# Kernel tuning notes

Measured on AMD Instinct MI355X. Metric: run time of the kernel, lower is better.

The kernel has to match this reference:

```python
import jax, jax.numpy as jnp
import numpy as np
from jax import lax

PATCH_NUM = 84      # MultiHeadSelector default
SCALE = 0.7         # scaling_factor for non-selected patches
KERNEL = jnp.array([[1., 2., 1.], [2., 4., 2.], [1., 2., 1.]], dtype=jnp.float32).reshape(1, 1, 3, 3)


def setup_inputs() -> dict:
    key = jax.random.key(0)
    k1, k2, k3, k4 = jax.random.split(key, 4)
    B, C, S, D = 8, 12, 784, 768   # batch, heads, patches (28x28), hidden
    N = S + 1
    hidden_states = jax.random.normal(k1, (B, N, D), jnp.float32)
    x = jax.random.normal(k2, (B, C, N, N), jnp.float32)          # attention weights
    s1 = 1.0 / np.sqrt(512).astype(np.float32)
    s2 = 1.0 / np.sqrt(D).astype(np.float32)
    gcn_w1 = jax.random.uniform(k3, (2, 512), jnp.float32, -s1, s1)
    gcn_w2 = jax.random.uniform(k4, (512, D), jnp.float32, -s2, s2)
    return {"hidden_states": hidden_states, "x": x, "gcn_w1": gcn_w1, "gcn_w2": gcn_w2, "select_num": 42}


def reference(hidden_states, x, gcn_w1, gcn_w2, select_num):
    B, C, N = x.shape[0], x.shape[1], x.shape[2]
    S = N - 1
    H = int(np.sqrt(S))
    # ---- top-k patch selection per head, rescale non-selected scores ----
    score = x[:, :, 0, 1:]                                   # [B,C,S] CLS->patch attn
    _, sel_idx = lax.top_k(score, PATCH_NUM)                 # [B,C,K]
    bi = jnp.arange(B)[:, None, None]
    ci = jnp.arange(C)[None, :, None]
    select = jnp.zeros(score.shape, bool).at[bi, ci, sel_idx].set(True)
    new_score = jnp.where(select, score, score * SCALE)
    amap = new_score.reshape(B, C, H, H)                     # attention map
    # ---- RelativeCoordPredictor ----
    m = amap.sum(axis=1).reshape(B, S)
    binary = (m > m.mean(axis=1, keepdims=True)).astype(amap.dtype)
    masked = (amap * binary.reshape(B, 1, H, H)).reshape(B, C, S).transpose(0, 2, 1)  # [B,S,C]
    anchor_idx = jnp.argmax(masked.mean(axis=-1), axis=-1)   # [B]
    ii, jj = jnp.meshgrid(jnp.arange(H), jnp.arange(H), indexing='ij')
    label = jnp.stack([ii, jj], -1).reshape(S, 2).astype(amap.dtype)  # [S,2] (i,j) coords
    anchor = label[anchor_idx]                               # [B,2]
    rc = (label[None, :, :] - anchor[:, None, :]) / H
    dist = jnp.sqrt((rc ** 2).sum(-1))
    ang = (jnp.arctan2(rc[:, :, 1], rc[:, :, 0]) / np.pi + 1.0) / 2.0
    structure_info = jnp.stack([dist, ang], -1)              # [B,S,2]
    pw = amap.reshape(B, C, S).transpose(0, 2, 1).mean(-1)   # [B,S]
    adj = pw[:, :, None] * pw[:, None, :]                    # [B,S,S] position weight
    # ---- GCN (eval mode; dropout off). relu(leaky_relu(x)) == relu(x). ----
    h1 = jnp.maximum(jnp.einsum('bst,btk->bsk', adj, structure_info @ gcn_w1), 0)
    o2 = jnp.einsum('bst,btk->bsk', adj, h1 @ gcn_w2)
    struct = jnp.where(o2 > 0, o2, 0.2 * o2)                 # [B,S,D]
    # ---- per-sample anchor injection into CLS token ----
    hs = hidden_states.at[:, 0].add(struct[jnp.arange(B), anchor_idx])
    # ---- vote counts across heads (bincount), local 3x3 enhancement ----
    count = jnp.zeros((B, S), hs.dtype).at[jnp.arange(B)[:, None], sel_idx.reshape(B, -1)].add(1.0)
    count = lax.conv_general_dilated(count.reshape(B, 1, H, H), KERNEL.astype(hs.dtype), (1, 1), 'SAME',
                                     dimension_numbers=('NCHW', 'OIHW', 'NCHW')).reshape(B, S)
    order = jnp.argsort(-count, axis=-1, stable=True)        # descending sort
    patch_idx = order[:, :select_num] + 1                    # +1 skips CLS token
    selected = hs[jnp.arange(B)[:, None], patch_idx]         # [B,select_num,D]
    return hs, selected
```

## Files before the change

### kernel.cpp

```cpp
#include <hip/hip_runtime.h>
#include <math.h>

#define Bz 8
#define Cc 12
#define Ss 784
#define Nn 785
#define Dd 768
#define Hh 28
#define K1 512
#define PATCHNUM 84

__device__ inline float waveSum(float v) {
#pragma unroll
    for (int off = 32; off > 0; off >>= 1) v += __shfl_xor(v, off);
    return v;
}

__global__ __launch_bounds__(256) void kA_score(const float* __restrict__ x,
                                                float* __restrict__ nscore,
                                                unsigned char* __restrict__ flags) {
    int bc = blockIdx.x;
    int quarter = blockIdx.y;
    int tid = threadIdx.x;
    const float* sc = x + (size_t)bc * Nn * Nn + 1;
    __shared__ float s_sc[Ss];
    for (int s = tid; s < Ss; s += 256) s_sc[s] = sc[s];
    __syncthreads();

    int s = tid + 256 * quarter;
    bool valid = (s < Ss);
    float v = valid ? s_sc[s] : 0.f;
    int rank = 0;
    const float4* s4 = (const float4*)s_sc;
    for (int chunk = 0; chunk < Ss / 16; ++chunk) {
        float4 c0 = s4[chunk * 4 + 0];
        float4 c1 = s4[chunk * 4 + 1];
        float4 c2 = s4[chunk * 4 + 2];
        float4 c3 = s4[chunk * 4 + 3];
        float c[16] = {c0.x, c0.y, c0.z, c0.w, c1.x, c1.y, c1.z, c1.w,
                       c2.x, c2.y, c2.z, c2.w, c3.x, c3.y, c3.z, c3.w};
#pragma unroll
        for (int u = 0; u < 16; ++u) {
            int t = chunk * 16 + u;
            rank += (c[u] > v) || (c[u] == v && t < s);
        }
    }
    if (valid) {
        bool sel = rank < PATCHNUM;
        flags[(size_t)bc * Ss + s] = sel ? 1 : 0;
        nscore[(size_t)bc * Ss + s] = sel ? v : v * 0.7f;
    }
}

__global__ __launch_bounds__(256) void kMid(const float* __restrict__ nscore,
                                            const unsigned char* __restrict__ flags,
                                            const float* __restrict__ w1,
                                            const float* __restrict__ w2,
                                            float* __restrict__ pbuf,
                                            int* __restrict__ selpos, int select_num) {
    int bid = blockIdx.x;
    int tid = threadIdx.x;
    int wid = tid >> 6, lane = tid & 63;

    if (bid < 192) {
        int b = bid / 24;
        int r = bid % 24;
        int kb = r / 3, colblk = r % 3;
        __shared__ float s_m[Ss];
        __shared__ float s_pw[Ss];
        __shared__ float s_g[64];
        __shared__ float s_w1[4];
        __shared__ float s_w4[4][4];
        __shared__ float s_av[4];
        __shared__ int   s_ai[4];

        const float* ns = nscore + (size_t)b * Cc * Ss;
        float lsum = 0.f;
        for (int s = tid; s < Ss; s += 256) {
            float m = 0.f;
#pragma unroll
            for (int c = 0; c < Cc; ++c) m += ns[c * Ss + s];
            s_m[s] = m;
            s_pw[s] = m / 12.0f;
            lsum += m;
        }
        lsum = waveSum(lsum);
        if (lane == 0) s_w1[wid] = lsum;
        __syncthreads();
        float meanm = (s_w1[0] + s_w1[1] + s_w1[2] + s_w1[3]) / 784.0f;

        float bv = -INFINITY; int bi = Ss;
        for (int s = tid; s < Ss; s += 256) {
            float z = (s_m[s] > meanm) ? s_pw[s] : 0.0f;
            if (z > bv) { bv = z; bi = s; }
        }
#pragma unroll
        for (int off = 32; off > 0; off >>= 1) {
            float ov = __shfl_xor(bv, off);
            int   oi = __shfl_xor(bi, off);
            if (ov > bv || (ov == bv && oi < bi)) { bv = ov; bi = oi; }
        }
        if (lane == 0) { s_av[wid] = bv; s_ai[wid] = bi; }
        __syncthreads();
        float abv = s_av[0]; int anchor = s_ai[0];
#pragma unroll
        for (int w = 1; w < 4; ++w) {
            if (s_av[w] > abv || (s_av[w] == abv && s_ai[w] < anchor)) {
                abv = s_av[w]; anchor = s_ai[w];
            }
        }

        int ai = anchor / Hh, aj = anchor % Hh;
        float lA = 0.f, lG = 0.f, lp = 0.f, ln2 = 0.f;
        const float PI_F = 3.14159265358979323846f;
        for (int s = tid; s < Ss; s += 256) {
            float pw = s_pw[s];
            int i = s / Hh, j = s % Hh;
            float ri = (float)(i - ai) / 28.0f;
            float rj = (float)(j - aj) / 28.0f;
            float dist = sqrtf(ri * ri + rj * rj);
            float ang = (atan2f(rj, ri) / PI_F + 1.0f) * 0.5f;
            lA += pw * dist;
            lG += pw * ang;
            if (pw > 0.f) lp += pw * pw;
            else if (pw < 0.f) ln2 += pw * pw;
        }
        lA = waveSum(lA); lG = waveSum(lG); lp = waveSum(lp); ln2 = waveSum(ln2);
        if (lane == 0) {
            s_w4[wid][0] = lA; s_w4[wid][1] = lG; s_w4[wid][2] = lp; s_w4[wid][3] = ln2;
        }
        __syncthreads();
        float A   = s_w4[0][0] + s_w4[1][0] + s_w4[2][0] + s_w4[3][0];
        float G   = s_w4[0][1] + s_w4[1][1] + s_w4[2][1] + s_w4[3][1];
        float P2p = s_w4[0][2] + s_w4[1][2] + s_w4[2][2] + s_w4[3][2];
        float P2n = s_w4[0][3] + s_w4[1][3] + s_w4[2][3] + s_w4[3][3];
        float pwA = s_pw[anchor];
        float cp = pwA * P2p, cn = pwA * P2n;

        if (tid < 64) {
            int k = kb * 64 + tid;
            float v = A * w1[k] + G * w1[K1 + k];
            s_g[tid] = cp * fmaxf(v, 0.f) - cn * fmaxf(-v, 0.f);
        }
        __syncthreads();

        int col = colblk * 256 + tid;
        float acc = 0.f;
        const float* w2p = w2 + (size_t)(kb * 64) * Dd + col;
#pragma unroll 8
        for (int kk = 0; kk < 64; ++kk)
            acc += s_g[kk] * w2p[kk * Dd];
        pbuf[((size_t)kb * Bz + b) * Dd + col] = acc;
    } else {
        int u = bid - 192;
        int b = u / 4;
        int quarter = u % 4;
        __shared__ int s_cnt[Ss];
        __shared__ int s_cc[Ss];
        for (int s = tid; s < Ss; s += 256) {
            int c0 = 0;
#pragma unroll
            for (int c = 0; c < Cc; ++c) c0 += flags[((size_t)b * Cc + c) * Ss + s];
            s_cnt[s] = c0;
        }
        __syncthreads();
        for (int s = tid; s < Ss; s += 256) {
            int i = s / Hh, j = s % Hh;
            int acc = 0;
            for (int di = -1; di <= 1; ++di)
                for (int dj = -1; dj <= 1; ++dj) {
                    int ii = i + di, jj = j + dj;
                    if (ii >= 0 && ii < Hh && jj >= 0 && jj < Hh)
                        acc += ((di == 0) ? 2 : 1) * ((dj == 0) ? 2 : 1) * s_cnt[ii * Hh + jj];
                }
            s_cc[s] = acc;
        }
        __syncthreads();
        int s = tid + 256 * quarter;
        int v = 0, rank = 0;
        bool valid = (s < Ss);
        if (valid) v = s_cc[s];
        const int4* s4 = (const int4*)s_cc;
        for (int chunk = 0; chunk < Ss / 16; ++chunk) {
            int4 c0 = s4[chunk * 4 + 0];
            int4 c1 = s4[chunk * 4 + 1];
            int4 c2 = s4[chunk * 4 + 2];
            int4 c3 = s4[chunk * 4 + 3];
            int c[16] = {c0.x, c0.y, c0.z, c0.w, c1.x, c1.y, c1.z, c1.w,
                         c2.x, c2.y, c2.z, c2.w, c3.x, c3.y, c3.z, c3.w};
#pragma unroll
            for (int u2 = 0; u2 < 16; ++u2) {
                int t = chunk * 16 + u2;
                rank += (c[u2] > v) || (c[u2] == v && t < s);
            }
        }
        if (valid && rank < select_num)
            selpos[b * select_num + rank] = s + 1;
    }
}

__global__ __launch_bounds__(256) void kE_out(const float* __restrict__ hs,
                                              const float* __restrict__ pbuf,
                                              const int* __restrict__ selpos,
                                              float* __restrict__ out,
                                              int select_num, int blocksCopy) {
    int bid = blockIdx.x;
    if (bid < blocksCopy) {
        size_t v = (size_t)bid * 256 + threadIdx.x;
        size_t total = (size_t)Bz * Nn * Dd / 4;
        if (v >= total) return;
        float4 val = ((const float4*)hs)[v];
        size_t fidx = v * 4;
        int b = (int)(fidx / ((size_t)Nn * Dd));
        int r = (int)(fidx % ((size_t)Nn * Dd));
        if (r < Dd) {
            float4 o2 = make_float4(0.f, 0.f, 0.f, 0.f);
#pragma unroll
            for (int kb = 0; kb < 8; ++kb) {
                float4 p = *(const float4*)(pbuf + ((size_t)kb * Bz + b) * Dd + r);
                o2.x += p.x; o2.y += p.y; o2.z += p.z; o2.w += p.w;
            }
            val.x += (o2.x > 0.f) ? o2.x : 0.2f * o2.x;
            val.y += (o2.y > 0.f) ? o2.y : 0.2f * o2.y;
            val.z += (o2.z > 0.f) ? o2.z : 0.2f * o2.z;
            val.w += (o2.w > 0.f) ? o2.w : 0.2f * o2.w;
        }
        ((float4*)out)[v] = val;
    } else {
        int v = (bid - blocksCopy) * 256 + threadIdx.x;
        int total = Bz * select_num * Dd / 4;
        if (v >= total) return;
        int fidx = v * 4;
        int b = fidx / (select_num * Dd);
        int r = fidx % (select_num * Dd);
        int p = r / Dd;
        int d = r % Dd;
        int row = selpos[b * select_num + p];
        float4 val = *(const float4*)(hs + ((size_t)b * Nn + row) * Dd + d);
        ((float4*)(out + (size_t)Bz * Nn * Dd))[v] = val;
    }
}

extern "C" void kernel_launch(void* const* d_in, const int* in_sizes, int n_in,
                              void* d_out, int out_size, void* d_ws, size_t ws_size,
                              hipStream_t stream) {
    const float* hs = (const float*)d_in[0];
    const float* x  = (const float*)d_in[1];
    const float* w1 = (const float*)d_in[2];
    const float* w2 = (const float*)d_in[3];
    float* out = (float*)d_out;

    const int hsN = Bz * Nn * Dd;
    int select_num = (out_size - hsN) / (Bz * Dd);

    char* ws = (char*)d_ws;
    float* nscore = (float*)ws;
    unsigned char* flags = (unsigned char*)(ws + 301056);
    float* pbuf  = (float*)(ws + 376320);
    int* selpos  = (int*)(ws + 572928);

    kA_score<<<dim3(Bz * Cc, 4), 256, 0, stream>>>(x, nscore, flags);
    kMid<<<224, 256, 0, stream>>>(nscore, flags, w1, w2, pbuf, selpos, select_num);

    int blocksCopy = (hsN / 4 + 255) / 256;
    int selTotal = Bz * select_num * Dd / 4;
    int blocksGather = (selTotal + 255) / 256;
    kE_out<<<blocksCopy + blocksGather, 256, 0, stream>>>(hs, pbuf, selpos, out,
                                                          select_num, blocksCopy);
}
```

Measured before the change: 54.46 us.

## Fuse all stages into one kernel with radix-select top-k and redundant per-block recomputation

Merges the three kernels into a single launch. Per-head top-84 is now found with a 4-pass 8-bit radix select in shared memory instead of an O(S^2) rank count. Each GCN block recomputes the top-k for all 12 heads of its batch and writes CLS+struct directly, and the vote/sort blocks do their own gather. The remaining blocks copy the non-CLS rows of hidden_states. This removes launch gaps and intermediate workspace traffic, at the cost of redundant top-k work: every block repeats all 12 heads serially, which lengthens the critical path of the compute blocks.

```diff
diff --git a/kernel.cpp b/kernel.cpp
--- a/kernel.cpp
+++ b/kernel.cpp
@@ -10,88 +10,189 @@
 #define K1 512
 #define PATCHNUM 84
 
+#define GRP1 96
+#define GRP2 16
+#define NCOPY 1200
+#define NBLK (GRP1 + GRP2 + NCOPY)
+
 __device__ inline float waveSum(float v) {
 #pragma unroll
     for (int off = 32; off > 0; off >>= 1) v += __shfl_xor(v, off);
     return v;
 }
 
-__global__ __launch_bounds__(256) void kA_score(const float* __restrict__ x,
-                                                float* __restrict__ nscore,
-                                                unsigned char* __restrict__ flags) {
-    int bc = blockIdx.x;
-    int quarter = blockIdx.y;
-    int tid = threadIdx.x;
-    const float* sc = x + (size_t)bc * Nn * Nn + 1;
-    __shared__ float s_sc[Ss];
-    for (int s = tid; s < Ss; s += 256) s_sc[s] = sc[s];
+__device__ inline unsigned int okey(float v) {
+    unsigned int u = __float_as_uint(v);
+    return (u & 0x80000000u) ? ~u : (u | 0x80000000u);
+}
+
+__device__ void topk84(float* s_val, unsigned int* s_key, int* s_hist,
+                       unsigned char* s_sel, unsigned long long* s_eq,
+                       unsigned int* st, int tid) {
+    const int lane = tid & 63;
+    const int wid = tid >> 6;
+    for (int s = tid; s < Ss; s += 256) s_key[s] = okey(s_val[s]);
+    if (tid == 0) { st[0] = PATCHNUM; st[2] = 0; st[3] = 0; st[8] = 0; }
     __syncthreads();
 
-    int s = tid + 256 * quarter;
-    bool valid = (s < Ss);
-    float v = valid ? s_sc[s] : 0.f;
-    int rank = 0;
-    const float4* s4 = (const float4*)s_sc;
-    for (int chunk = 0; chunk < Ss / 16; ++chunk) {
-        float4 c0 = s4[chunk * 4 + 0];
-        float4 c1 = s4[chunk * 4 + 1];
-        float4 c2 = s4[chunk * 4 + 2];
-        float4 c3 = s4[chunk * 4 + 3];
-        float c[16] = {c0.x, c0.y, c0.z, c0.w, c1.x, c1.y, c1.z, c1.w,
-                       c2.x, c2.y, c2.z, c2.w, c3.x, c3.y, c3.z, c3.w};
-#pragma unroll
-        for (int u = 0; u < 16; ++u) {
-            int t = chunk * 16 + u;
-            rank += (c[u] > v) || (c[u] == v && t < s);
-        }
+    for (int pass = 0; pass < 4; ++pass) {
+        unsigned int rem = st[0], pfx = st[2], nb = st[3], have = st[8];
+        if (have) break;
+        s_hist[tid] = 0;
+        __syncthreads();
+        int shiftP = 8 * (3 - pass);
+        for (int s = tid; s < Ss; s += 256) {
+            unsigned int k = s_key[s];
+            bool match = (nb == 0) ? true : ((k >> (8 * (4 - nb))) == pfx);
+            if (match) atomicAdd(&s_hist[(k >> shiftP) & 255u], 1);
+        }
+        __syncthreads();
+        if (tid < 64) {
+            int base = tid << 2;
+            int h0 = s_hist[base + 0], h1 = s_hist[base + 1];
+            int h2 = s_hist[base + 2], h3 = s_hist[base + 3];
+            int loc = h0 + h1 + h2 + h3;
+            int suf = loc;
+#pragma unroll
+            for (int off = 1; off < 64; off <<= 1) {
+                int o = __shfl_down(suf, off);
+                if (tid + off < 64) suf += o;
+            }
+            int excl = suf - loc;
+            int remi = (int)rem;
+            int hh[4] = {h3, h2, h1, h0};
+#pragma unroll
+            for (int j = 0; j < 4; ++j) {
+                int inc = excl + hh[j];
+                if (excl < remi && remi <= inc) {
+                    st[4] = (unsigned int)(base + 3 - j);
+                    st[5] = (unsigned int)excl;
+                    st[6] = (unsigned int)hh[j];
+                }
+                excl = inc;
+            }
+        }
+        __syncthreads();
+        unsigned int B = st[4], excl = st[5], histB = st[6];
+        unsigned int npfx = (pfx << 8) | B;
+        unsigned int nnb = nb + 1;
+        bool last = (pass == 3);
+        bool uniq = (histB == 1u) && !last;
+        if (uniq) {
+            for (int s = tid; s < Ss; s += 256) {
+                unsigned int k = s_key[s];
+                if ((k >> (8 * (4 - nnb))) == npfx) st[7] = k;
+            }
+        }
+        if (tid == 0) {
+            st[0] = rem - excl;
+            st[2] = npfx;
+            st[3] = nnb;
+            if (last) st[7] = npfx;
+            st[8] = (last || uniq) ? 1u : 0u;
+        }
+        __syncthreads();
     }
-    if (valid) {
-        bool sel = rank < PATCHNUM;
-        flags[(size_t)bc * Ss + s] = sel ? 1 : 0;
-        nscore[(size_t)bc * Ss + s] = sel ? v : v * 0.7f;
+
+    unsigned int T = st[7];
+    int quota = (int)st[0];
+    for (int s = tid; s < Ss; s += 256) s_sel[s] = (s_key[s] > T) ? 1 : 0;
+    for (int q = 0; q < 4; ++q) {
+        int s = q * 256 + wid * 64 + lane;
+        bool eqv = (s < Ss) && (s_key[s] == T);
+        unsigned long long msk = __ballot(eqv);
+        int strip = q * 4 + wid;
+        if (lane == 0 && strip < 13) s_eq[strip] = msk;
     }
-}
-
-__global__ __launch_bounds__(256) void kMid(const float* __restrict__ nscore,
-                                            const unsigned char* __restrict__ flags,
-                                            const float* __restrict__ w1,
-                                            const float* __restrict__ w2,
-                                            float* __restrict__ pbuf,
-                                            int* __restrict__ selpos, int select_num) {
+    __syncthreads();
+    if (tid == 0) {
+        int need = quota;
+        for (int strip = 0; strip < 13 && need > 0; ++strip) {
+            unsigned long long msk = s_eq[strip];
+            while (msk && need > 0) {
+                int bpos = __ffsll(msk) - 1;
+                s_sel[strip * 64 + bpos] = 1;
+                msk &= msk - 1;
+                --need;
+            }
+        }
+    }
+    __syncthreads();
+}
+
+struct G1 {
+    float val[Ss];
+    unsigned int key[Ss];
+    int hist[256];
+    unsigned char sel[Ss];
+    unsigned long long eq[13];
+    unsigned int st[12];
+    float m[Ss];
+    float pw[Ss];
+    float g[K1];
+    float part[4][64];
+    float w4[4][4];
+    float av[4];
+    int ai4[4];
+    float w1s[4];
+};
+struct G2 {
+    float val[Ss];
+    unsigned int key[Ss];
+    int hist[256];
+    unsigned char sel[Ss];
+    unsigned long long eq[13];
+    unsigned int st[12];
+    int cnt[Ss];
+    int cc[Ss];
+    int found[64];
+};
+union SMem { G1 g1; G2 g2; };
+
+__global__ __launch_bounds__(256) void kFused(const float* __restrict__ hs,
+                                              const float* __restrict__ x,
+                                              const float* __restrict__ w1,
+                                              const float* __restrict__ w2,
+                                              float* __restrict__ out,
+                                              int select_num) {
+    __shared__ SMem sm;
     int bid = blockIdx.x;
     int tid = threadIdx.x;
-    int wid = tid >> 6, lane = tid & 63;
-
-    if (bid < 192) {
-        int b = bid / 24;
-        int r = bid % 24;
-        int kb = r / 3, colblk = r % 3;
-        __shared__ float s_m[Ss];
-        __shared__ float s_pw[Ss];
-        __shared__ float s_g[64];
-        __shared__ float s_w1[4];
-        __shared__ float s_w4[4][4];
-        __shared__ float s_av[4];
-        __shared__ int   s_ai[4];
-
-        const float* ns = nscore + (size_t)b * Cc * Ss;
+    int lane = tid & 63, wid = tid >> 6;
+
+    if (bid < GRP1) {
+        G1& S = sm.g1;
+        int b = bid / 12;
+        int colblk = bid % 12;
+
+        for (int s = tid; s < Ss; s += 256) S.m[s] = 0.f;
+        __syncthreads();
+        for (int c = 0; c < Cc; ++c) {
+            const float* xs = x + (size_t)(b * Cc + c) * Nn * Nn + 1;
+            for (int s = tid; s < Ss; s += 256) S.val[s] = xs[s];
+            __syncthreads();
+            topk84(S.val, S.key, S.hist, S.sel, S.eq, S.st, tid);
+            for (int s = tid; s < Ss; s += 256) {
+                float v = S.val[s];
+                S.m[s] += S.sel[s] ? v : 0.7f * v;
+            }
+            __syncthreads();
+        }
+
         float lsum = 0.f;
         for (int s = tid; s < Ss; s += 256) {
-            float m = 0.f;
-#pragma unroll
-            for (int c = 0; c < Cc; ++c) m += ns[c * Ss + s];
-            s_m[s] = m;
-            s_pw[s] = m / 12.0f;
-            lsum += m;
+            float mm = S.m[s];
+            S.pw[s] = mm / 12.0f;
+            lsum += mm;
         }
         lsum = waveSum(lsum);
-        if (lane == 0) s_w1[wid] = lsum;
-        __syncthreads();
-        float meanm = (s_w1[0] + s_w1[1] + s_w1[2] + s_w1[3]) / 784.0f;
+        if (lane == 0) S.w1s[wid] = lsum;
+        __syncthreads();
+        float meanm = (S.w1s[0] + S.w1s[1] + S.w1s[2] + S.w1s[3]) / 784.0f;
 
         float bv = -INFINITY; int bi = Ss;
         for (int s = tid; s < Ss; s += 256) {
-            float z = (s_m[s] > meanm) ? s_pw[s] : 0.0f;
+            float z = (S.m[s] > meanm) ? S.pw[s] : 0.0f;
             if (z > bv) { bv = z; bi = s; }
         }
 #pragma unroll
@@ -100,13 +201,13 @@
             int   oi = __shfl_xor(bi, off);
             if (ov > bv || (ov == bv && oi < bi)) { bv = ov; bi = oi; }
         }
-        if (lane == 0) { s_av[wid] = bv; s_ai[wid] = bi; }
-        __syncthreads();
-        float abv = s_av[0]; int anchor = s_ai[0];
+        if (lane == 0) { S.av[wid] = bv; S.ai4[wid] = bi; }
+        __syncthreads();
+        float abv = S.av[0]; int anchor = S.ai4[0];
 #pragma unroll
         for (int w = 1; w < 4; ++w) {
-            if (s_av[w] > abv || (s_av[w] == abv && s_ai[w] < anchor)) {
-                abv = s_av[w]; anchor = s_ai[w];
+            if (S.av[w] > abv || (S.av[w] == abv && S.ai4[w] < anchor)) {
+                abv = S.av[w]; anchor = S.ai4[w];
             }
         }
 
@@ -114,7 +215,7 @@
         float lA = 0.f, lG = 0.f, lp = 0.f, ln2 = 0.f;
         const float PI_F = 3.14159265358979323846f;
         for (int s = tid; s < Ss; s += 256) {
-            float pw = s_pw[s];
+            float pw = S.pw[s];
             int i = s / Hh, j = s % Hh;
             float ri = (float)(i - ai) / 28.0f;
             float rj = (float)(j - aj) / 28.0f;
@@ -127,43 +228,53 @@
         }
         lA = waveSum(lA); lG = waveSum(lG); lp = waveSum(lp); ln2 = waveSum(ln2);
         if (lane == 0) {
-            s_w4[wid][0] = lA; s_w4[wid][1] = lG; s_w4[wid][2] = lp; s_w4[wid][3] = ln2;
-        }
-        __syncthreads();
-        float A   = s_w4[0][0] + s_w4[1][0] + s_w4[2][0] + s_w4[3][0];
-        float G   = s_w4[0][1] + s_w4[1][1] + s_w4[2][1] + s_w4[3][1];
-        float P2p = s_w4[0][2] + s_w4[1][2] + s_w4[2][2] + s_w4[3][2];
-        float P2n = s_w4[0][3] + s_w4[1][3] + s_w4[2][3] + s_w4[3][3];
-        float pwA = s_pw[anchor];
+            S.w4[wid][0] = lA; S.w4[wid][1] = lG; S.w4[wid][2] = lp; S.w4[wid][3] = ln2;
+        }
+        __syncthreads();
+        float A   = S.w4[0][0] + S.w4[1][0] + S.w4[2][0] + S.w4[3][0];
+        float G   = S.w4[0][1] + S.w4[1][1] + S.w4[2][1] + S.w4[3][1];
+        float P2p = S.w4[0][2] + S.w4[1][2] + S.w4[2][2] + S.w4[3][2];
+        float P2n = S.w4[0][3] + S.w4[1][3] + S.w4[2][3] + S.w4[3][3];
+        float pwA = S.pw[anchor];
         float cp = pwA * P2p, cn = pwA * P2n;
 
+        for (int k = tid; k < K1; k += 256) {
+            float v = A * w1[k] + G * w1[K1 + k];
+            S.g[k] = cp * fmaxf(v, 0.f) - cn * fmaxf(-v, 0.f);
+        }
+        __syncthreads();
+
+        int col = colblk * 64 + (tid & 63);
+        int kc = tid >> 6;
+        float acc = 0.f;
+        const float* w2p = w2 + (size_t)(kc * 128) * Dd + col;
+#pragma unroll 8
+        for (int kk = 0; kk < 128; ++kk)
+            acc += S.g[kc * 128 + kk] * w2p[kk * Dd];
+        S.part[kc][tid & 63] = acc;
+        __syncthreads();
         if (tid < 64) {
-            int k = kb * 64 + tid;
-            float v = A * w1[k] + G * w1[K1 + k];
-            s_g[tid] = cp * fmaxf(v, 0.f) - cn * fmaxf(-v, 0.f);
-        }
-        __syncthreads();
-
-        int col = colblk * 256 + tid;
-        float acc = 0.f;
-        const float* w2p = w2 + (size_t)(kb * 64) * Dd + col;
-#pragma unroll 8
-        for (int kk = 0; kk < 64; ++kk)
-            acc += s_g[kk] * w2p[kk * Dd];
-        pbuf[((size_t)kb * Bz + b) * Dd + col] = acc;
-    } else {
-        int u = bid - 192;
-        int b = u / 4;
-        int quarter = u % 4;
-        __shared__ int s_cnt[Ss];
-        __shared__ int s_cc[Ss];
-        for (int s = tid; s < Ss; s += 256) {
-            int c0 = 0;
-#pragma unroll
-            for (int c = 0; c < Cc; ++c) c0 += flags[((size_t)b * Cc + c) * Ss + s];
-            s_cnt[s] = c0;
-        }
-        __syncthreads();
+            float o2 = S.part[0][tid] + S.part[1][tid] + S.part[2][tid] + S.part[3][tid];
+            float r = (o2 > 0.f) ? o2 : 0.2f * o2;
+            size_t off = (size_t)b * Nn * Dd + colblk * 64 + tid;
+            out[off] = hs[off] + r;
+        }
+    } else if (bid < GRP1 + GRP2) {
+        G2& S = sm.g2;
+        int u = bid - GRP1;
+        int b = u >> 1, half = u & 1;
+
+        for (int s = tid; s < Ss; s += 256) S.cnt[s] = 0;
+        for (int r = tid; r < 64; r += 256) S.found[r] = -1;
+        __syncthreads();
+        for (int c = 0; c < Cc; ++c) {
+            const float* xs = x + (size_t)(b * Cc + c) * Nn * Nn + 1;
+            for (int s = tid; s < Ss; s += 256) S.val[s] = xs[s];
+            __syncthreads();
+            topk84(S.val, S.key, S.hist, S.sel, S.eq, S.st, tid);
+            for (int s = tid; s < Ss; s += 256) S.cnt[s] += S.sel[s];
+            __syncthreads();
+        }
         for (int s = tid; s < Ss; s += 256) {
             int i = s / Hh, j = s % Hh;
             int acc = 0;
@@ -171,73 +282,54 @@
                 for (int dj = -1; dj <= 1; ++dj) {
                     int ii = i + di, jj = j + dj;
                     if (ii >= 0 && ii < Hh && jj >= 0 && jj < Hh)
-                        acc += ((di == 0) ? 2 : 1) * ((dj == 0) ? 2 : 1) * s_cnt[ii * Hh + jj];
+                        acc += ((di == 0) ? 2 : 1) * ((dj == 0) ? 2 : 1) * S.cnt[ii * Hh + jj];
                 }
-            s_cc[s] = acc;
-        }
-        __syncthreads();
-        int s = tid + 256 * quarter;
-        int v = 0, rank = 0;
-        bool valid = (s < Ss);
-        if (valid) v = s_cc[s];
-        const int4* s4 = (const int4*)s_cc;
-        for (int chunk = 0; chunk < Ss / 16; ++chunk) {
-            int4 c0 = s4[chunk * 4 + 0];
-            int4 c1 = s4[chunk * 4 + 1];
-            int4 c2 = s4[chunk * 4 + 2];
-            int4 c3 = s4[chunk * 4 + 3];
+            S.cc[s] = acc;
+        }
+        __syncthreads();
+
+        int sA = half * 392 + tid;
+        int sB = (tid < 136) ? (half * 392 + 256 + tid) : -1;
+        int vA = S.cc[sA];
+        int vB = (sB >= 0) ? S.cc[sB] : 0;
+        int rA = 0, rB = 0;
+        const int4* p4 = (const int4*)S.cc;
+        for (int ch = 0; ch < 49; ++ch) {
+            int4 c0 = p4[ch * 4 + 0];
+            int4 c1 = p4[ch * 4 + 1];
+            int4 c2 = p4[ch * 4 + 2];
+            int4 c3 = p4[ch * 4 + 3];
             int c[16] = {c0.x, c0.y, c0.z, c0.w, c1.x, c1.y, c1.z, c1.w,
                          c2.x, c2.y, c2.z, c2.w, c3.x, c3.y, c3.z, c3.w};
 #pragma unroll
             for (int u2 = 0; u2 < 16; ++u2) {
-                int t = chunk * 16 + u2;
-                rank += (c[u2] > v) || (c[u2] == v && t < s);
-            }
-        }
-        if (valid && rank < select_num)
-            selpos[b * select_num + rank] = s + 1;
-    }
-}
-
-__global__ __launch_bounds__(256) void kE_out(const float* __restrict__ hs,
-                                              const float* __restrict__ pbuf,
-                                              const int* __restrict__ selpos,
-                                              float* __restrict__ out,
-                                              int select_num, int blocksCopy) {
-    int bid = blockIdx.x;
-    if (bid < blocksCopy) {
-        size_t v = (size_t)bid * 256 + threadIdx.x;
-        size_t total = (size_t)Bz * Nn * Dd / 4;
-        if (v >= total) return;
-        float4 val = ((const float4*)hs)[v];
-        size_t fidx = v * 4;
-        int b = (int)(fidx / ((size_t)Nn * Dd));
-        int r = (int)(fidx % ((size_t)Nn * Dd));
-        if (r < Dd) {
-            float4 o2 = make_float4(0.f, 0.f, 0.f, 0.f);
-#pragma unroll
-            for (int kb = 0; kb < 8; ++kb) {
-                float4 p = *(const float4*)(pbuf + ((size_t)kb * Bz + b) * Dd + r);
-                o2.x += p.x; o2.y += p.y; o2.z += p.z; o2.w += p.w;
-            }
-            val.x += (o2.x > 0.f) ? o2.x : 0.2f * o2.x;
-            val.y += (o2.y > 0.f) ? o2.y : 0.2f * o2.y;
-            val.z += (o2.z > 0.f) ? o2.z : 0.2f * o2.z;
-            val.w += (o2.w > 0.f) ? o2.w : 0.2f * o2.w;
-        }
-        ((float4*)out)[v] = val;
+                int t = ch * 16 + u2;
+                rA += (c[u2] > vA) || (c[u2] == vA && t < sA);
+                rB += (c[u2] > vB) || (c[u2] == vB && t < sB);
+            }
+        }
+        if (rA < select_num && rA < 64) S.found[rA] = sA + 1;
+        if (sB >= 0 && rB < select_num && rB < 64) S.found[rB] = sB + 1;
+        __syncthreads();
+
+        for (int r = 0; r < select_num; ++r) {
+            int src = S.found[r];
+            if (src < 0) continue;
+            const float4* sp = (const float4*)(hs + ((size_t)b * Nn + src) * Dd);
+            float4* dp = (float4*)(out + (size_t)Bz * Nn * Dd + ((size_t)b * select_num + r) * Dd);
+            if (tid < Dd / 4) dp[tid] = sp[tid];
+        }
     } else {
-        int v = (bid - blocksCopy) * 256 + threadIdx.x;
-        int total = Bz * select_num * Dd / 4;
-        if (v >= total) return;
-        int fidx = v * 4;
-        int b = fidx / (select_num * Dd);
-        int r = fidx % (select_num * Dd);
-        int p = r / Dd;
-        int d = r % Dd;
-        int row = selpos[b * select_num + p];
-        float4 val = *(const float4*)(hs + ((size_t)b * Nn + row) * Dd + d);
-        ((float4*)(out + (size_t)Bz * Nn * Dd))[v] = val;
+        const size_t totalF4 = (size_t)Bz * Ss * Dd / 4;
+        const size_t perB   = (size_t)Ss * Dd / 4;
+        const size_t rowPit = (size_t)Nn * Dd / 4;
+        size_t f = (size_t)(bid - GRP1 - GRP2) * 256 + tid;
+        for (; f < totalF4; f += (size_t)NCOPY * 256) {
+            size_t b = f / perB;
+            size_t r = f - b * perB;
+            size_t idx = b * rowPit + (Dd / 4) + r;
+            ((float4*)out)[idx] = ((const float4*)hs)[idx];
+        }
     }
 }
 
@@ -253,18 +345,5 @@
     const int hsN = Bz * Nn * Dd;
     int select_num = (out_size - hsN) / (Bz * Dd);
 
-    char* ws = (char*)d_ws;
-    float* nscore = (float*)ws;
-    unsigned char* flags = (unsigned char*)(ws + 301056);
-    float* pbuf  = (float*)(ws + 376320);
-    int* selpos  = (int*)(ws + 572928);
-
-    kA_score<<<dim3(Bz * Cc, 4), 256, 0, stream>>>(x, nscore, flags);
-    kMid<<<224, 256, 0, stream>>>(nscore, flags, w1, w2, pbuf, selpos, select_num);
-
-    int blocksCopy = (hsN / 4 + 255) / 256;
-    int selTotal = Bz * select_num * Dd / 4;
-    int blocksGather = (selTotal + 255) / 256;
-    kE_out<<<blocksCopy + blocksGather, 256, 0, stream>>>(hs, pbuf, selpos, out,
-                                                          select_num, blocksCopy);
-}
+    kFused<<<NBLK, 256, 0, stream>>>(hs, x, w1, w2, out, select_num);
+}
```

New measurement: 132.0 us. 142% more time.
